# Kernel tuning notes

Hardware: AMD Instinct MI355X
Metric: run time of the kernel (lower is better)

## Reference

```python
import jax, jax.numpy as jnp
import numpy as np

NEG = -1e12


def setup_inputs() -> dict:
    key = jax.random.key(0)
    ks = jax.random.split(key, 10)
    B, C, Q, D = 16, 384, 64, 2048
    return {
        "c": jax.random.normal(ks[0], (B, C, D), dtype=jnp.float32),
        "q": jax.random.normal(ks[1], (B, Q, D), dtype=jnp.float32),
        "c_len": jax.random.randint(ks[2], (B,), 1, C + 1),
        "q_len": jax.random.randint(ks[3], (B,), 1, Q + 1),
        "w_c": jax.random.normal(ks[4], (D,), dtype=jnp.float32) * 0.02,
        "b_c": jnp.zeros((), dtype=jnp.float32),
        "w_q": jax.random.normal(ks[5], (D,), dtype=jnp.float32) * 0.02,
        "b_q": jnp.zeros((), dtype=jnp.float32),
        "w_cq": jax.random.normal(ks[6], (D,), dtype=jnp.float32) * 0.02,
        "b_cq": jnp.zeros((), dtype=jnp.float32),
        "W_out": jax.random.normal(ks[7], (4 * D, 2), dtype=jnp.float32) * 0.02,
        "b_out": jnp.zeros((2,), dtype=jnp.float32),
    }


def reference(c, q, c_len, q_len, w_c, b_c, w_q, b_q, w_cq, b_cq, W_out, b_out):
    B, C, D = c.shape
    Q = q.shape[1]
    # trilinear similarity: s[b,r,i] = w_c.c_r + w_q.q_i + w_cq.(c_r*q_i) + biases
    cq = jnp.einsum('bcd,bqd,d->bcq', c, q, w_cq) + b_cq          # [B,C,Q]
    s = (c @ w_c + b_c)[:, :, None] + (q @ w_q + b_q)[:, None, :] + cq
    rows = jnp.arange(C)[None, :, None]
    cols = jnp.arange(Q)[None, None, :]
    # faithful to the triple loop: cols >= q_len OR (rows >= c_len AND col < Q-1)
    masked = (cols >= q_len[:, None, None]) | (
        (rows >= c_len[:, None, None]) & (cols < Q - 1))
    s = s + jnp.where(masked, jnp.float32(NEG), jnp.float32(0.0))
    a = jax.nn.softmax(s, axis=2)                                  # [B,C,Q]
    c2q = jnp.einsum('bcq,bqd->bcd', a, q)                         # [B,C,D]
    b_att = jax.nn.softmax(jnp.max(s, axis=2), axis=1)             # [B,C]
    q2c = jnp.einsum('bc,bcd->bd', b_att, c)[:, None, :]           # [B,1,D]
    x = jnp.concatenate(
        [c, c2q, c * c2q, c * jnp.broadcast_to(q2c, c.shape)], axis=-1)
    out = x @ W_out + b_out                                        # [B,C,2]
    # final masking: out[i][c_len[i]:-1] = NEG (last row untouched)
    row_mask = (jnp.arange(C)[None, :] >= c_len[:, None]) & (
        jnp.arange(C)[None, :] < C - 1)
    out = jnp.where(row_mask[..., None], jnp.float32(NEG), out)
    return out[..., 0], out[..., 1]
```

## Files before the change

kernel.cpp:

```cpp
#include <hip/hip_runtime.h>

#define NEGV -1.0e12f
constexpr int B = 16, C = 384, Q = 64, D = 2048;
constexpr int PITCH = 40;
constexpr int IST = 8320;
constexpr int NIMG = 64;
constexpr int NT = 96;
constexpr int KC = 4;
constexpr int SP = 208;

typedef __attribute__((ext_vector_type(8))) short s16x8;
typedef __attribute__((ext_vector_type(4))) float f32x4;

__device__ __forceinline__ unsigned pkbf(float lo, float hi) {
  unsigned ulo = __builtin_bit_cast(unsigned, lo);
  unsigned uhi = __builtin_bit_cast(unsigned, hi);
  return (uhi & 0xFFFF0000u) | (ulo >> 16);
}
__device__ __forceinline__ float bflo(unsigned u) {
  return __builtin_bit_cast(float, u << 16);
}
__device__ __forceinline__ float bfhi(unsigned u) {
  return __builtin_bit_cast(float, u & 0xFFFF0000u);
}
__device__ __forceinline__ float bfs(unsigned short u) {
  return __builtin_bit_cast(float, ((unsigned)u) << 16);
}

#define GLD_LDS(gsrc, ldst)                                              \
  __builtin_amdgcn_global_load_lds(                                      \
      (const __attribute__((address_space(1))) unsigned*)(gsrc),         \
      (__attribute__((address_space(3))) unsigned*)(ldst), 16, 0, 0)

__global__ __launch_bounds__(256) void k_pq(
    const float* __restrict__ q, const float* __restrict__ w_cq,
    const float* __restrict__ w_c, const float* __restrict__ w_q,
    const float* __restrict__ W_out, unsigned short* __restrict__ bpk,
    float* __restrict__ qstats) {
  const int t = threadIdx.x;
  if (blockIdx.x < 512) {
    const int s = blockIdx.x & 31, b = blockIdx.x >> 5;
    const int k0 = s * 64;
    unsigned short* base = bpk + (size_t)b * NIMG * IST;
#pragma unroll
    for (int i = 0; i < 4; ++i) {
      int idx = t + 256 * i;
      int qi = idx >> 4, kc = (idx & 15) * 4;
      unsigned short* img = base + (size_t)(s * 2 + (kc >> 5)) * IST;
      const int ko = kc & 31;
      float4 qv = *(const float4*)(q + ((size_t)b * Q + qi) * D + k0 + kc);
      float4 wq = *(const float4*)(w_cq + k0 + kc);
      const float* wp = W_out + (size_t)(2 * D + k0 + kc) * 2;
      float4 wa = *(const float4*)(wp);
      float4 wb = *(const float4*)(wp + 4);
      uint2 u;
      u.x = pkbf(qv.x * wq.x, qv.y * wq.y);
      u.y = pkbf(qv.z * wq.z, qv.w * wq.w);
      *(uint2*)(img + qi * PITCH + ko) = u;
      u.x = pkbf(qv.x * wa.x, qv.y * wa.z);
      u.y = pkbf(qv.z * wb.x, qv.w * wb.z);
      *(uint2*)(img + (64 + qi) * PITCH + ko) = u;
      u.x = pkbf(qv.x * wa.y, qv.y * wa.w);
      u.y = pkbf(qv.z * wb.y, qv.w * wb.w);
      *(uint2*)(img + (128 + qi) * PITCH + ko) = u;
    }
    if (t < 48) {
      int r = t >> 4, kc = (t & 15) * 4;
      unsigned short* img = base + (size_t)(s * 2 + (kc >> 5)) * IST;
      const int ko = kc & 31;
      uint2 u;
      if (r == 0) {
        float4 w = *(const float4*)(w_c + k0 + kc);
        u.x = pkbf(w.x, w.y);
        u.y = pkbf(w.z, w.w);
      } else {
        const float* wp = W_out + (size_t)(k0 + kc) * 2 + (r - 1);
        u.x = pkbf(wp[0], wp[2]);
        u.y = pkbf(wp[4], wp[6]);
      }
      *(uint2*)(img + (192 + r) * PITCH + ko) = u;
    }
  } else {
    int bi = blockIdx.x - 512;
    const float* qrow = q + (size_t)bi * D;
    float a0 = 0.f, a1 = 0.f, a2 = 0.f;
    for (int d = t * 4; d < D; d += 256 * 4) {
      float4 qv = *(const float4*)(qrow + d);
      float4 wq = *(const float4*)(w_q + d);
      const float* wp = W_out + (size_t)(D + d) * 2;
      float4 wa = *(const float4*)(wp);
      float4 wb = *(const float4*)(wp + 4);
      a0 += qv.x * wq.x + qv.y * wq.y + qv.z * wq.z + qv.w * wq.w;
      a1 += qv.x * wa.x + qv.y * wa.z + qv.z * wb.x + qv.w * wb.z;
      a2 += qv.x * wa.y + qv.y * wa.w + qv.z * wb.y + qv.w * wb.w;
    }
    for (int m = 1; m < 64; m <<= 1) {
      a0 += __shfl_xor(a0, m, 64);
      a1 += __shfl_xor(a1, m, 64);
      a2 += __shfl_xor(a2, m, 64);
    }
    __shared__ float red[3][4];
    int w = t >> 6, lane = t & 63;
    if (lane == 0) { red[0][w] = a0; red[1][w] = a1; red[2][w] = a2; }
    __syncthreads();
    if (t == 0) {
      qstats[bi * 3 + 0] = red[0][0] + red[0][1] + red[0][2] + red[0][3];
      qstats[bi * 3 + 1] = red[1][0] + red[1][1] + red[1][2] + red[1][3];
      qstats[bi * 3 + 2] = red[2][0] + red[2][1] + red[2][2] + red[2][3];
    }
  }
}

__global__ __launch_bounds__(512, 1) void k_score(
    const unsigned short* __restrict__ bpk, const float* __restrict__ c,
    unsigned short* __restrict__ S3pb, unsigned short* __restrict__ cbf) {
  const int t = threadIdx.x;
  const int lane = t & 63, wv = t >> 6;
  const int bid = blockIdx.x;
  const int b = bid & 15, kcb = (bid >> 4) & 3, n0 = (bid >> 6) * NT;
  const int lr = lane & 15, lg = lane >> 4;
  const int mg = wv >> 1, ng = wv & 1;

  __shared__ unsigned short sBp[4][IST];
  __shared__ unsigned short sCp[4][NT * PITCH];

  const unsigned short* gB = bpk + ((size_t)b * NIMG + kcb * 16) * IST;
  const float* cbase = c + ((size_t)b * C + n0) * D + kcb * 512;
  unsigned short* cbf_base = cbf + ((size_t)b * C + n0) * D + kcb * 512;

  f32x4 acc[4][3];
#pragma unroll
  for (int f = 0; f < 4; ++f)
#pragma unroll
    for (int g = 0; g < 3; ++g) acc[f][g] = f32x4{0.f, 0.f, 0.f, 0.f};

  auto stageB = [&](int buf, int s) {
    const char* src = (const char*)gB + (size_t)s * (IST * 2);
    char* dst = (char*)&sBp[buf][0];
    GLD_LDS(src + t * 16, dst + t * 16);
    GLD_LDS(src + 8192 + t * 16, dst + 8192 + t * 16);
    if (t < 16) GLD_LDS(src + 16384 + t * 16, dst + 16384 + t * 16);
  };
  auto loadC = [&](float4* r, int s) {
    const float* base = cbase + s * 32;
    if (wv < 4) {
      int g0 = wv * 128 + lane;
      r[0] = *(const float4*)(base + (size_t)(g0 >> 3) * D + (g0 & 7) * 4);
      int g1 = g0 + 64;
      r[1] = *(const float4*)(base + (size_t)(g1 >> 3) * D + (g1 & 7) * 4);
    } else {
      int g0 = 512 + (wv - 4) * 64 + lane;
      r[0] = *(const float4*)(base + (size_t)(g0 >> 3) * D + (g0 & 7) * 4);
    }
  };
  auto writeC = [&](int buf, const float4* r, int s) {
    unsigned short* cb = cbf_base + s * 32;
    if (wv < 4) {
      int g0 = wv * 128 + lane;
      uint2 u0 = {pkbf(r[0].x, r[0].y), pkbf(r[0].z, r[0].w)};
      *(uint2*)&sCp[buf][(g0 >> 3) * PITCH + (g0 & 7) * 4] = u0;
      *(uint2*)(cb + (size_t)(g0 >> 3) * D + (g0 & 7) * 4) = u0;
      int g1 = g0 + 64;
      uint2 u1 = {pkbf(r[1].x, r[1].y), pkbf(r[1].z, r[1].w)};
      *(uint2*)&sCp[buf][(g1 >> 3) * PITCH + (g1 & 7) * 4] = u1;
      *(uint2*)(cb + (size_t)(g1 >> 3) * D + (g1 & 7) * 4) = u1;
    } else {
      int g0 = 512 + (wv - 4) * 64 + lane;
      uint2 u0 = {pkbf(r[0].x, r[0].y), pkbf(r[0].z, r[0].w)};
      *(uint2*)&sCp[buf][(g0 >> 3) * PITCH + (g0 & 7) * 4] = u0;
      *(uint2*)(cb + (size_t)(g0 >> 3) * D + (g0 & 7) * 4) = u0;
    }
  };
  auto compute = [&](int buf) {
    s16x8 af[4], bf[3];
#pragma unroll
    for (int f = 0; f < 4; ++f)
      af[f] = *(const s16x8*)&sBp[buf][(mg * 64 + f * 16 + lr) * PITCH +
                                       lg * 8];
#pragma unroll
    for (int g = 0; g < 3; ++g)
      bf[g] = *(const s16x8*)&sCp[buf][((ng * 3 + g) * 16 + lr) * PITCH +
                                       lg * 8];
#pragma unroll
    for (int f = 0; f < 4; ++f)
#pragma unroll
      for (int g = 0; g < 3; ++g)
        acc[f][g] =
            __builtin_amdgcn_mfma_f32_16x16x32_bf16(af[f], bf[g], acc[f][g],
                                                    0, 0, 0);
  };

  auto vmwait2 = [&]() {
    if (wv == 0)
      asm volatile("s_waitcnt vmcnt(14)" ::: "memory");
    else if (wv < 4)
      asm volatile("s_waitcnt vmcnt(12)" ::: "memory");
    else
      asm volatile("s_waitcnt vmcnt(8)" ::: "memory");
  };
  auto vmwait1 = [&]() {
    if (wv == 0)
      asm volatile("s_waitcnt vmcnt(7)" ::: "memory");
    else if (wv < 4)
      asm volatile("s_waitcnt vmcnt(6)" ::: "memory");
    else
      asm volatile("s_waitcnt vmcnt(4)" ::: "memory");
  };

  float4 rc[4][2];
  stageB(0, 0);
  loadC(rc[0], 0);
  stageB(1, 1);
  loadC(rc[1], 1);
#pragma unroll
  for (int s = 0; s < 16; ++s) {
    const int cur = s & 3;
    if (s + 2 < 16) {
      stageB((s + 2) & 3, s + 2);
      loadC(rc[(s + 2) & 3], s + 2);
      vmwait2();
    } else if (s + 1 < 16) {
      vmwait1();
    } else {
      asm volatile("s_waitcnt vmcnt(0)" ::: "memory");
    }
    writeC(cur, rc[cur], s);
    asm volatile("s_waitcnt lgkmcnt(0)" ::: "memory");
    __builtin_amdgcn_sched_barrier(0);
    __builtin_amdgcn_s_barrier();
    compute(cur);
  }

  const size_t rowbase = ((size_t)kcb * B + b) * C;
#pragma unroll
  for (int f = 0; f < 4; ++f) {
    int mf = mg * 4 + f;
    if (mf < 13) {
#pragma unroll
      for (int g = 0; g < 3; ++g) {
        int n = n0 + (ng * 3 + g) * 16 + lr;
        uint2 pk;
        pk.x = pkbf(acc[f][g][0], acc[f][g][1]);
        pk.y = pkbf(acc[f][g][2], acc[f][g][3]);
        *(uint2*)(S3pb + (rowbase + n) * SP + mf * 16 + lg * 4) = pk;
      }
    }
  }
}

__global__ __launch_bounds__(256) void k_soft(
    const unsigned short* __restrict__ S3pb, const float* __restrict__ qstats,
    const int* __restrict__ c_len, const int* __restrict__ q_len,
    const float* __restrict__ b_c, const float* __restrict__ b_q,
    const float* __restrict__ b_cq, float* __restrict__ mrow,
    float* __restrict__ out12) {
  const int t = threadIdx.x, lane = t & 63;
  const int rg = blockIdx.x * 4 + (t >> 6);
  const int b = rg / C, r = rg % C;
  float s_cq = 0.f, sc = 0.f, w10 = 0.f, w11 = 0.f, t30 = 0.f, t31 = 0.f;
#pragma unroll
  for (int p = 0; p < KC; ++p) {
    const unsigned short* Sr = S3pb + ((size_t)p * B * C + rg) * SP;
    s_cq += bfs(Sr[lane]);
    sc += bfs(Sr[192]);
    w10 += bfs(Sr[193]);
    w11 += bfs(Sr[194]);
    t30 += bfs(Sr[64 + lane]);
    t31 += bfs(Sr[128 + lane]);
  }
  const float qs0 = qstats[((b << 6) + lane) * 3 + 0];
  const float qs1 = qstats[((b << 6) + lane) * 3 + 1];
  const float qs2 = qstats[((b << 6) + lane) * 3 + 2];
  float s = s_cq + sc + qs0 + b_c[0] + b_q[0] + b_cq[0];
  const int cl = c_len[b], ql = q_len[b];
  bool masked = (lane >= ql) || ((r >= cl) && (lane < Q - 1));
  if (masked) s += NEGV;
  float mx = s;
  for (int m = 1; m < 64; m <<= 1) mx = fmaxf(mx, __shfl_xor(mx, m, 64));
  float e = __expf(s - mx);
  float den = e;
  for (int m = 1; m < 64; m <<= 1) den += __shfl_xor(den, m, 64);
  float a = e / den;
  float v0 = a * (qs1 + t30);
  float v1 = a * (qs2 + t31);
  for (int m = 1; m < 64; m <<= 1) {
    v0 += __shfl_xor(v0, m, 64);
    v1 += __shfl_xor(v1, m, 64);
  }
  if (lane == 0) {
    mrow[rg] = mx;
    out12[rg * 2 + 0] = w10 + v0;
    out12[rg * 2 + 1] = w11 + v1;
  }
}

__global__ __launch_bounds__(512) void k_q2cu(
    const unsigned short* __restrict__ cbf, const float* __restrict__ mrow,
    const float* __restrict__ W_out, float* __restrict__ uvec) {
  const int ch = blockIdx.x, b = blockIdx.y;
  const int t = threadIdx.x, lane = t & 63, wv = t >> 6;
  __shared__ float batt[C];
  __shared__ float rmx[8], rsm[8];
  __shared__ float redq0[8][64], redq1[8][64];

  float m = (t < C) ? mrow[b * C + t] : -3.0e38f;
  float mx = m;
  for (int o = 1; o < 64; o <<= 1) mx = fmaxf(mx, __shfl_xor(mx, o, 64));
  if (lane == 0) rmx[wv] = mx;
  __syncthreads();
  mx = rmx[0];
#pragma unroll
  for (int i = 1; i < 8; ++i) mx = fmaxf(mx, rmx[i]);
  float e = (t < C) ? __expf(m - mx) : 0.f;
  float sm = e;
  for (int o = 1; o < 64; o <<= 1) sm += __shfl_xor(sm, o, 64);
  if (lane == 0) rsm[wv] = sm;
  __syncthreads();
  sm = rsm[0] + rsm[1] + rsm[2] + rsm[3] + rsm[4] + rsm[5] + rsm[6] + rsm[7];
  if (t < C) batt[t] = e / sm;
  __syncthreads();

  const int d0 = ch * 128 + lane * 2;
  const unsigned short* p = cbf + ((size_t)b * C + wv * 8) * D + d0;
  float A0[8] = {0.f, 0.f, 0.f, 0.f, 0.f, 0.f, 0.f, 0.f};
  float A1[8] = {0.f, 0.f, 0.f, 0.f, 0.f, 0.f, 0.f, 0.f};
#pragma unroll
  for (int r0 = 0; r0 < 384; r0 += 64) {
    const unsigned short* pr = p + (size_t)r0 * D;
    const float* bt = &batt[r0 + wv * 8];
#pragma unroll
    for (int j = 0; j < 8; ++j) {
      unsigned cc = *(const unsigned*)(pr + (size_t)j * D);
      A0[j] += bt[j] * bflo(cc);
      A1[j] += bt[j] * bfhi(cc);
    }
  }
  float s0 = ((A0[0] + A0[1]) + (A0[2] + A0[3])) +
             ((A0[4] + A0[5]) + (A0[6] + A0[7]));
  float s1 = ((A1[0] + A1[1]) + (A1[2] + A1[3])) +
             ((A1[4] + A1[5]) + (A1[6] + A1[7]));
  redq0[wv][lane] = s0;
  redq1[wv][lane] = s1;
  __syncthreads();
  if (t < 64) {
    float q0 = 0.f, q1 = 0.f;
#pragma unroll
    for (int w = 0; w < 8; ++w) {
      q0 += redq0[w][t];
      q1 += redq1[w][t];
    }
    int dd = ch * 128 + t * 2;
    float4 w4 = *(const float4*)(W_out + (size_t)(3 * D + dd) * 2);
    float4 u = {q0 * w4.x, q0 * w4.y, q1 * w4.z, q1 * w4.w};
    *(float4*)(uvec + ((size_t)b * D + dd) * 2) = u;
  }
}

__global__ __launch_bounds__(512) void k_out(
    const unsigned short* __restrict__ cbf, const float* __restrict__ uvec,
    const float* __restrict__ out12, const float* __restrict__ b_out,
    const int* __restrict__ c_len, float* __restrict__ outp) {
  const int b = blockIdx.y, r0 = blockIdx.x * 8;
  const int t = threadIdx.x, lane = t & 63, wv = t >> 6;
  __shared__ float u_sh[2 * D];

  {
    const float* src = uvec + (size_t)b * D * 2 + t * 8;
    float4 v0 = *(const float4*)(src);
    float4 v1 = *(const float4*)(src + 4);
    *(float4*)&u_sh[t * 8] = v0;
    *(float4*)&u_sh[t * 8 + 4] = v1;
  }
  __syncthreads();

  const int r = r0 + wv;
  const unsigned short* crow = cbf + ((size_t)b * C + r) * D;
  float o0 = 0.f, o1 = 0.f;
#pragma unroll
  for (int it = 0; it < 16; ++it) {
    int d0 = it * 128 + lane * 2;
    unsigned cc = *(const unsigned*)(crow + d0);
    float c0 = bflo(cc), c1 = bfhi(cc);
    float4 u = *(const float4*)&u_sh[d0 * 2];
    o0 += c0 * u.x + c1 * u.z;
    o1 += c0 * u.y + c1 * u.w;
  }
  for (int o = 1; o < 64; o <<= 1) {
    o0 += __shfl_xor(o0, o, 64);
    o1 += __shfl_xor(o1, o, 64);
  }
  if (lane == 0) {
    const int idx = b * C + r;
    o0 += out12[idx * 2 + 0] + b_out[0];
    o1 += out12[idx * 2 + 1] + b_out[1];
    if (r >= c_len[b] && r < C - 1) { o0 = NEGV; o1 = NEGV; }
    outp[idx] = o0;
    outp[B * C + idx] = o1;
  }
}

extern "C" void kernel_launch(void* const* d_in, const int* in_sizes, int n_in,
                              void* d_out, int out_size, void* d_ws,
                              size_t ws_size, hipStream_t stream) {
  const float* c = (const float*)d_in[0];
  const float* q = (const float*)d_in[1];
  const int* c_len = (const int*)d_in[2];
  const int* q_len = (const int*)d_in[3];
  const float* w_c = (const float*)d_in[4];
  const float* b_c = (const float*)d_in[5];
  const float* w_q = (const float*)d_in[6];
  const float* b_q = (const float*)d_in[7];
  const float* w_cq = (const float*)d_in[8];
  const float* b_cq = (const float*)d_in[9];
  const float* W_out = (const float*)d_in[10];
  const float* b_out = (const float*)d_in[11];
  float* outp = (float*)d_out;

  unsigned short* bpk = (unsigned short*)d_ws;
  const size_t bpk_bytes = (size_t)B * NIMG * IST * 2;
  unsigned short* S3pb = (unsigned short*)((char*)d_ws + bpk_bytes);
  const size_t s3_elems = (size_t)KC * B * C * SP;
  float* ws = (float*)(S3pb + s3_elems);
  float* qstats = ws;
  float* mrow = ws + 3072;
  float* out12 = ws + 3072 + 6144;
  float* uvec = ws + 3072 + 6144 + 12288;
  unsigned short* cbf = (unsigned short*)(uvec + 65536);

  hipLaunchKernelGGL(k_pq, dim3(512 + B * Q), dim3(256), 0, stream, q, w_cq,
                     w_c, w_q, W_out, bpk, qstats);
  hipLaunchKernelGGL(k_score, dim3(4 * KC * B), dim3(512), 0, stream, bpk, c,
                     S3pb, cbf);
  hipLaunchKernelGGL(k_soft, dim3(B * C / 4), dim3(256), 0, stream, S3pb,
                     qstats, c_len, q_len, b_c, b_q, b_cq, mrow, out12);
  hipLaunchKernelGGL(k_q2cu, dim3(16, B), dim3(512), 0, stream, cbf, mrow,
                     W_out, uvec);
  hipLaunchKernelGGL(k_out, dim3(C / 8, B), dim3(512), 0, stream, cbf, uvec,
                     out12, b_out, c_len, outp);
}
```

Before: 47.27 us.

## Build packed q-weight B operand inside score kernel instead of prep kernel

The prep kernel no longer writes a large pre-packed bf16 image of q scaled by w_cq and W_out columns to global memory. It now writes only a small packed weight vector. The score kernel loads raw q in fp32, multiplies by the weights cached in LDS, and packs to bf16 directly into shared memory each stage. This removes a global write plus re-read of the packed image, at the cost of extra VALU work and extra LDS traffic inside the MFMA pipeline. The q tiles are now reloaded redundantly by the 4 column-tile blocks.

```diff
diff --git a/kernel.cpp b/kernel.cpp
--- a/kernel.cpp
+++ b/kernel.cpp
@@ -4,7 +4,6 @@
 constexpr int B = 16, C = 384, Q = 64, D = 2048;
 constexpr int PITCH = 40;
 constexpr int IST = 8320;
-constexpr int NIMG = 64;
 constexpr int NT = 96;
 constexpr int KC = 4;
 constexpr int SP = 208;
@@ -32,56 +31,14 @@
       (const __attribute__((address_space(1))) unsigned*)(gsrc),         \
       (__attribute__((address_space(3))) unsigned*)(ldst), 16, 0, 0)
 
-__global__ __launch_bounds__(256) void k_pq(
-    const float* __restrict__ q, const float* __restrict__ w_cq,
-    const float* __restrict__ w_c, const float* __restrict__ w_q,
-    const float* __restrict__ W_out, unsigned short* __restrict__ bpk,
-    float* __restrict__ qstats) {
+__global__ __launch_bounds__(256) void k_prep(
+    const float* __restrict__ q, const float* __restrict__ w_q,
+    const float* __restrict__ w_cq, const float* __restrict__ w_c,
+    const float* __restrict__ W_out, float* __restrict__ qstats,
+    float* __restrict__ wpack) {
   const int t = threadIdx.x;
-  if (blockIdx.x < 512) {
-    const int s = blockIdx.x & 31, b = blockIdx.x >> 5;
-    const int k0 = s * 64;
-    unsigned short* base = bpk + (size_t)b * NIMG * IST;
-#pragma unroll
-    for (int i = 0; i < 4; ++i) {
-      int idx = t + 256 * i;
-      int qi = idx >> 4, kc = (idx & 15) * 4;
-      unsigned short* img = base + (size_t)(s * 2 + (kc >> 5)) * IST;
-      const int ko = kc & 31;
-      float4 qv = *(const float4*)(q + ((size_t)b * Q + qi) * D + k0 + kc);
-      float4 wq = *(const float4*)(w_cq + k0 + kc);
-      const float* wp = W_out + (size_t)(2 * D + k0 + kc) * 2;
-      float4 wa = *(const float4*)(wp);
-      float4 wb = *(const float4*)(wp + 4);
-      uint2 u;
-      u.x = pkbf(qv.x * wq.x, qv.y * wq.y);
-      u.y = pkbf(qv.z * wq.z, qv.w * wq.w);
-      *(uint2*)(img + qi * PITCH + ko) = u;
-      u.x = pkbf(qv.x * wa.x, qv.y * wa.z);
-      u.y = pkbf(qv.z * wb.x, qv.w * wb.z);
-      *(uint2*)(img + (64 + qi) * PITCH + ko) = u;
-      u.x = pkbf(qv.x * wa.y, qv.y * wa.w);
-      u.y = pkbf(qv.z * wb.y, qv.w * wb.w);
-      *(uint2*)(img + (128 + qi) * PITCH + ko) = u;
-    }
-    if (t < 48) {
-      int r = t >> 4, kc = (t & 15) * 4;
-      unsigned short* img = base + (size_t)(s * 2 + (kc >> 5)) * IST;
-      const int ko = kc & 31;
-      uint2 u;
-      if (r == 0) {
-        float4 w = *(const float4*)(w_c + k0 + kc);
-        u.x = pkbf(w.x, w.y);
-        u.y = pkbf(w.z, w.w);
-      } else {
-        const float* wp = W_out + (size_t)(k0 + kc) * 2 + (r - 1);
-        u.x = pkbf(wp[0], wp[2]);
-        u.y = pkbf(wp[4], wp[6]);
-      }
-      *(uint2*)(img + (192 + r) * PITCH + ko) = u;
-    }
-  } else {
-    int bi = blockIdx.x - 512;
+  if (blockIdx.x < 1024) {
+    int bi = blockIdx.x;
     const float* qrow = q + (size_t)bi * D;
     float a0 = 0.f, a1 = 0.f, a2 = 0.f;
     for (int d = t * 4; d < D; d += 256 * 4) {
@@ -108,12 +65,35 @@
       qstats[bi * 3 + 1] = red[1][0] + red[1][1] + red[1][2] + red[1][3];
       qstats[bi * 3 + 2] = red[2][0] + red[2][1] + red[2][2] + red[2][3];
     }
+  } else {
+    int wb = blockIdx.x - 1024;
+    int plane = wb >> 1, half = wb & 1;
+    int k = half * 1024 + t * 4;
+    float4 v;
+    if (plane == 0) {
+      v = *(const float4*)(w_cq + k);
+    } else if (plane == 3) {
+      v = *(const float4*)(w_c + k);
+    } else {
+      const float* s;
+      if (plane == 1)
+        s = W_out + (size_t)(2 * D + k) * 2;
+      else if (plane == 2)
+        s = W_out + (size_t)(2 * D + k) * 2 + 1;
+      else if (plane == 4)
+        s = W_out + (size_t)k * 2;
+      else
+        s = W_out + (size_t)k * 2 + 1;
+      v = make_float4(s[0], s[2], s[4], s[6]);
+    }
+    *(float4*)(wpack + plane * 2048 + k) = v;
   }
 }
 
 __global__ __launch_bounds__(512, 1) void k_score(
-    const unsigned short* __restrict__ bpk, const float* __restrict__ c,
-    unsigned short* __restrict__ S3pb, unsigned short* __restrict__ cbf) {
+    const float* __restrict__ wpack, const float* __restrict__ q,
+    const float* __restrict__ c, unsigned short* __restrict__ S3pb,
+    unsigned short* __restrict__ cbf) {
   const int t = threadIdx.x;
   const int lane = t & 63, wv = t >> 6;
   const int bid = blockIdx.x;
@@ -123,10 +103,24 @@
 
   __shared__ unsigned short sBp[4][IST];
   __shared__ unsigned short sCp[4][NT * PITCH];
-
-  const unsigned short* gB = bpk + ((size_t)b * NIMG + kcb * 16) * IST;
+  __shared__ float wL[6 * 512];
+
+  {
+    int p = t >> 7, j4 = (t & 127) * 4;
+    GLD_LDS(wpack + p * 2048 + kcb * 512 + j4, wL + p * 512 + j4);
+    if (t < 256) {
+      int c2 = 512 + t;
+      int p2 = c2 >> 7, k4 = (c2 & 127) * 4;
+      GLD_LDS(wpack + p2 * 2048 + kcb * 512 + k4, wL + p2 * 512 + k4);
+    }
+  }
+  asm volatile("s_waitcnt vmcnt(0)" ::: "memory");
+  __builtin_amdgcn_s_barrier();
+
   const float* cbase = c + ((size_t)b * C + n0) * D + kcb * 512;
   unsigned short* cbf_base = cbf + ((size_t)b * C + n0) * D + kcb * 512;
+  const int qi = t >> 3, qkc = (t & 7) * 4;
+  const float* qbase = q + ((size_t)b * Q + qi) * D + kcb * 512 + qkc;
 
   f32x4 acc[4][3];
 #pragma unroll
@@ -134,12 +128,8 @@
 #pragma unroll
     for (int g = 0; g < 3; ++g) acc[f][g] = f32x4{0.f, 0.f, 0.f, 0.f};
 
-  auto stageB = [&](int buf, int s) {
-    const char* src = (const char*)gB + (size_t)s * (IST * 2);
-    char* dst = (char*)&sBp[buf][0];
-    GLD_LDS(src + t * 16, dst + t * 16);
-    GLD_LDS(src + 8192 + t * 16, dst + 8192 + t * 16);
-    if (t < 16) GLD_LDS(src + 16384 + t * 16, dst + 16384 + t * 16);
+  auto loadQ = [&](float4& r, int s) {
+    r = *(const float4*)(qbase + s * 32);
   };
   auto loadC = [&](float4* r, int s) {
     const float* base = cbase + s * 32;
@@ -151,6 +141,30 @@
     } else {
       int g0 = 512 + (wv - 4) * 64 + lane;
       r[0] = *(const float4*)(base + (size_t)(g0 >> 3) * D + (g0 & 7) * 4);
+    }
+  };
+  auto writeB = [&](int buf, const float4& rq, int s) {
+    int ko = s * 32 + qkc;
+    float4 w0 = *(const float4*)&wL[ko];
+    float4 w1 = *(const float4*)&wL[512 + ko];
+    float4 w2 = *(const float4*)&wL[1024 + ko];
+    uint2 u;
+    u.x = pkbf(rq.x * w0.x, rq.y * w0.y);
+    u.y = pkbf(rq.z * w0.z, rq.w * w0.w);
+    *(uint2*)&sBp[buf][qi * PITCH + qkc] = u;
+    u.x = pkbf(rq.x * w1.x, rq.y * w1.y);
+    u.y = pkbf(rq.z * w1.z, rq.w * w1.w);
+    *(uint2*)&sBp[buf][(64 + qi) * PITCH + qkc] = u;
+    u.x = pkbf(rq.x * w2.x, rq.y * w2.y);
+    u.y = pkbf(rq.z * w2.z, rq.w * w2.w);
+    *(uint2*)&sBp[buf][(128 + qi) * PITCH + qkc] = u;
+    if (t < 24) {
+      int r = t >> 3, kc2 = (t & 7) * 4;
+      float4 wv4 = *(const float4*)&wL[(3 + r) * 512 + s * 32 + kc2];
+      uint2 us;
+      us.x = pkbf(wv4.x, wv4.y);
+      us.y = pkbf(wv4.z, wv4.w);
+      *(uint2*)&sBp[buf][(192 + r) * PITCH + kc2] = us;
     }
   };
   auto writeC = [&](int buf, const float4* r, int s) {
@@ -191,39 +205,42 @@
   };
 
   auto vmwait2 = [&]() {
-    if (wv == 0)
-      asm volatile("s_waitcnt vmcnt(14)" ::: "memory");
-    else if (wv < 4)
-      asm volatile("s_waitcnt vmcnt(12)" ::: "memory");
+    if (wv < 4)
+      asm volatile("s_waitcnt vmcnt(10)" ::: "memory");
     else
-      asm volatile("s_waitcnt vmcnt(8)" ::: "memory");
+      asm volatile("s_waitcnt vmcnt(6)" ::: "memory");
   };
   auto vmwait1 = [&]() {
-    if (wv == 0)
+    if (wv < 4)
       asm volatile("s_waitcnt vmcnt(7)" ::: "memory");
-    else if (wv < 4)
-      asm volatile("s_waitcnt vmcnt(6)" ::: "memory");
     else
       asm volatile("s_waitcnt vmcnt(4)" ::: "memory");
   };
-
-  float4 rc[4][2];
-  stageB(0, 0);
+  auto vmwait0 = [&]() {
+    if (wv < 4)
+      asm volatile("s_waitcnt vmcnt(4)" ::: "memory");
+    else
+      asm volatile("s_waitcnt vmcnt(2)" ::: "memory");
+  };
+
+  float4 rc[4][2], rq[4];
   loadC(rc[0], 0);
-  stageB(1, 1);
+  loadQ(rq[0], 0);
   loadC(rc[1], 1);
+  loadQ(rq[1], 1);
 #pragma unroll
   for (int s = 0; s < 16; ++s) {
     const int cur = s & 3;
     if (s + 2 < 16) {
-      stageB((s + 2) & 3, s + 2);
       loadC(rc[(s + 2) & 3], s + 2);
+      loadQ(rq[(s + 2) & 3], s + 2);
       vmwait2();
     } else if (s + 1 < 16) {
       vmwait1();
     } else {
-      asm volatile("s_waitcnt vmcnt(0)" ::: "memory");
-    }
+      vmwait0();
+    }
+    writeB(cur, rq[cur], s);
     writeC(cur, rc[cur], s);
     asm volatile("s_waitcnt lgkmcnt(0)" ::: "memory");
     __builtin_amdgcn_sched_barrier(0);
@@ -416,9 +433,8 @@
   const float* b_out = (const float*)d_in[11];
   float* outp = (float*)d_out;
 
-  unsigned short* bpk = (unsigned short*)d_ws;
-  const size_t bpk_bytes = (size_t)B * NIMG * IST * 2;
-  unsigned short* S3pb = (unsigned short*)((char*)d_ws + bpk_bytes);
+  float* wpack = (float*)d_ws;
+  unsigned short* S3pb = (unsigned short*)(wpack + 6 * 2048);
   const size_t s3_elems = (size_t)KC * B * C * SP;
   float* ws = (float*)(S3pb + s3_elems);
   float* qstats = ws;
@@ -427,10 +443,10 @@
   float* uvec = ws + 3072 + 6144 + 12288;
   unsigned short* cbf = (unsigned short*)(uvec + 65536);
 
-  hipLaunchKernelGGL(k_pq, dim3(512 + B * Q), dim3(256), 0, stream, q, w_cq,
-                     w_c, w_q, W_out, bpk, qstats);
-  hipLaunchKernelGGL(k_score, dim3(4 * KC * B), dim3(512), 0, stream, bpk, c,
-                     S3pb, cbf);
+  hipLaunchKernelGGL(k_prep, dim3(1024 + 12), dim3(256), 0, stream, q, w_q,
+                     w_cq, w_c, W_out, qstats, wpack);
+  hipLaunchKernelGGL(k_score, dim3(4 * KC * B), dim3(512), 0, stream, wpack,
+                     q, c, S3pb, cbf);
   hipLaunchKernelGGL(k_soft, dim3(B * C / 4), dim3(256), 0, stream, S3pb,
                      qstats, c_len, q_len, b_c, b_q, b_cq, mrow, out12);
   hipLaunchKernelGGL(k_q2cu, dim3(16, B), dim3(512), 0, stream, cbf, mrow,
```

After: 43.92 us (median of 2 runs). 1.08x faster.
